# Performance work log

Hardware: AMD Instinct MI355X
Metric: run time of the kernel (lower is better)

Reference implementation:

```python
import jax, jax.numpy as jnp
import numpy as np

NUM_LEVELS = 3
BASE_SCALE = 0.25
RES = 3
TRUNC_K = 128
KNN = 32
EPS = 1e-5


def group_norm(x, w, b, groups):
    # x: [B, C, *spatial]
    B, C = x.shape[0], x.shape[1]
    xr = x.reshape(B, groups, -1)
    m = xr.mean(-1, keepdims=True)
    v = xr.var(-1, keepdims=True)
    xn = ((xr - m) * jax.lax.rsqrt(v + EPS)).reshape(x.shape)
    bshape = (1, C) + (1,) * (x.ndim - 2)
    return xn * w.reshape(bshape) + b.reshape(bshape)


def prelu(x, a):
    return jnp.where(x >= 0, x, a * x)


def setup_inputs() -> dict:
    key = jax.random.key(0)
    ks = jax.random.split(key, 12)
    b, dim, n = 2, 128, 8192
    inp = {
        'fmap1': jax.random.normal(ks[0], (b, dim, n), jnp.float32),
        'fmap2': jax.random.normal(ks[1], (b, dim, n), jnp.float32),
        'xyz2': jax.random.normal(ks[2], (b, n, 3), jnp.float32),
        'coords': jax.random.normal(ks[3], (b, n, 3), jnp.float32),
        # out_conv: Conv1d(81,128,1) -> GN(8,128) -> PReLU -> Conv1d(128,64,1)
        'oc_w1': jax.random.normal(ks[4], (128, RES ** 3 * NUM_LEVELS), jnp.float32) * 0.05,
        'oc_b1': jnp.zeros((128,), jnp.float32),
        'oc_gn_w': jnp.ones((128,), jnp.float32),
        'oc_gn_b': jnp.zeros((128,), jnp.float32),
        'oc_prelu': jnp.asarray(0.25, jnp.float32),
        'oc_w2': jax.random.normal(ks[5], (64, 128), jnp.float32) * 0.05,
        'oc_b2': jnp.zeros((64,), jnp.float32),
        # knn_conv: Conv2d(4,64,1) -> GN(8,64) -> PReLU
        'kc_w': jax.random.normal(ks[6], (64, 4), jnp.float32) * 0.1,
        'kc_b': jnp.zeros((64,), jnp.float32),
        'kc_gn_w': jnp.ones((64,), jnp.float32),
        'kc_gn_b': jnp.zeros((64,), jnp.float32),
        'kc_prelu': jnp.asarray(0.25, jnp.float32),
        # knn_out: Conv1d(64,64,1)
        'ko_w': jax.random.normal(ks[7], (64, 64), jnp.float32) * 0.05,
        'ko_b': jnp.zeros((64,), jnp.float32),
    }
    return inp


def _forward(fmap1, fmap2, xyz2, coords,
             oc_w1, oc_b1, oc_gn_w, oc_gn_b, oc_prelu, oc_w2, oc_b2,
             kc_w, kc_b, kc_gn_w, kc_gn_b, kc_prelu, ko_w, ko_b):
    b, dim, n1 = fmap1.shape
    # --- init_module: correlation + top-k truncation ---
    corr = jnp.einsum('bdm,bdn->bmn', fmap1, fmap2) / jnp.sqrt(jnp.asarray(dim, jnp.float32))
    tcorr, idx = jax.lax.top_k(corr, TRUNC_K)           # [b,n1,K]
    txyz = jax.vmap(lambda pts, i: pts[i])(xyz2, idx)   # [b,n1,K,3]

    # --- voxel feature: per-level histogram scatter-add with count normalization ---
    half = np.floor(RES / 2)
    feats = []
    for lvl in range(NUM_LEVELS):
        r = BASE_SCALE * 2 ** lvl
        dv = jnp.round((txyz - coords[:, :, None, :]) / r)               # [b,n1,K,3]
        valid = jnp.all(jnp.abs(dv) <= half, axis=-1)                     # [b,n1,K] bool
        dv = dv + 1.0
        cube = (dv[..., 0] * RES ** 2 + dv[..., 1] * RES + dv[..., 2]).astype(jnp.int32)
        cube = jax.lax.stop_gradient(cube * valid)                        # invalid -> bin 0
        vmask = jax.lax.stop_gradient(valid.astype(tcorr.dtype))
        onehot = jax.nn.one_hot(cube, RES ** 3, dtype=tcorr.dtype)        # [b,n1,K,27]
        corr_add = jnp.einsum('bnk,bnkc->bnc', tcorr * vmask, onehot)
        corr_cnt = jnp.clip(jnp.einsum('bnk,bnkc->bnc', vmask, onehot), 1.0, float(n1))
        feats.append(jnp.transpose(corr_add / corr_cnt, (0, 2, 1)))       # [b,27,n1]
    vox = jnp.concatenate(feats, axis=1)                                  # [b,81,n1]
    h = jnp.einsum('oc,bcn->bon', oc_w1, vox) + oc_b1[None, :, None]
    h = prelu(group_norm(h, oc_gn_w, oc_gn_b, 8), oc_prelu)
    vox_feat = jnp.einsum('oc,bcn->bon', oc_w2, h) + oc_b2[None, :, None]  # [b,64,n1]

    # --- knn feature: nearest truncated correspondences, conv, max-pool ---
    diff = txyz - coords[:, :, None, :]
    dist = jnp.sum(diff * diff, axis=-1)                                  # [b,n1,K]
    _, nbr = jax.lax.top_k(-dist, KNN)                                    # [b,n1,knn]
    knn_corr = jnp.take_along_axis(tcorr, nbr, axis=2)[:, None]           # [b,1,n1,knn]
    knn_xyz = jnp.take_along_axis(txyz, nbr[..., None], axis=2)           # [b,n1,knn,3]
    knn_xyz = jnp.transpose(knn_xyz, (0, 3, 1, 2)) - jnp.transpose(coords, (0, 2, 1))[..., None]
    kin = jnp.concatenate([knn_corr, knn_xyz], axis=1)                    # [b,4,n1,knn]
    kf = jnp.einsum('oc,bcnk->bonk', kc_w, kin) + kc_b[None, :, None, None]
    kf = prelu(group_norm(kf, kc_gn_w, kc_gn_b, 8), kc_prelu)
    kf = jnp.max(kf, axis=3)                                              # [b,64,n1]
    knn_feat = jnp.einsum('oc,bcn->bon', ko_w, kf) + ko_b[None, :, None]

    return vox_feat + knn_feat                                            # [b,64,n1]


def reference(fmap1, fmap2, xyz2, coords,
              oc_w1, oc_b1, oc_gn_w, oc_gn_b, oc_prelu, oc_w2, oc_b2,
              kc_w, kc_b, kc_gn_w, kc_gn_b, kc_prelu, ko_w, ko_b):
    return _forward(fmap1, fmap2, xyz2, coords,
                    oc_w1, oc_b1, oc_gn_w, oc_gn_b, oc_prelu, oc_w2, oc_b2,
                    kc_w, kc_b, kc_gn_w, kc_gn_b, kc_prelu, ko_w, ko_b)
```

## Files before the change

### kernel.cpp

```cpp
#include <hip/hip_runtime.h>

#define NN 8192
#define TK 128
#define KNNK 32
#define CAP 352
#define CSTR 353

typedef unsigned long long u64;
typedef long long i64;
typedef unsigned int u32;
typedef unsigned short u16;
typedef _Float16 f16;
typedef __attribute__((ext_vector_type(8))) _Float16 half8;
typedef __attribute__((ext_vector_type(4))) float f32x4;


union HU { u16 u; f16 f; };
__device__ __forceinline__ u16 f2h_bits(float v){ HU h; h.f = (f16)v; return h.u; }
__device__ __forceinline__ float h2f(u16 u){ HU h; h.u = u; return (float)h.f; }

__device__ __forceinline__ u32 f2key(float v){
    u32 u = __float_as_uint(v);
    return u ^ ((u32)((int)u >> 31) | 0x80000000u);
}
__device__ __forceinline__ float key2f(u32 k){
    u32 u = (k & 0x80000000u) ? (k ^ 0x80000000u) : ~k;
    return __uint_as_float(u);
}

__global__ void k0_zero(u64* __restrict__ stats){
    const int t = threadIdx.x;
    if (t < 72) stats[t] = 0ull;
}

__global__ __launch_bounds__(256) void k0b_pack(const float* __restrict__ src,
                                                f16* __restrict__ pl){
    const int tid = blockIdx.x*256 + threadIdx.x;
    const int n  = tid & (NN-1);
    const int kg = (tid >> 13) & 15;
    const int b  = tid >> 17;
    const float* s = src + ((size_t)(b*128 + kg*8))*NN + n;
    u32 hw[4], lw[4];
    #pragma unroll
    for (int p=0; p<4; ++p){
        const float v0 = s[(2*p  )*NN], v1 = s[(2*p+1)*NN];
        const u16 h0 = f2h_bits(v0), h1 = f2h_bits(v1);
        const float r0 = (v0 - h2f(h0))*1024.f, r1 = (v1 - h2f(h1))*1024.f;
        hw[p] = (u32)h0 | ((u32)h1 << 16);
        lw[p] = (u32)f2h_bits(r0) | ((u32)f2h_bits(r1) << 16);
    }
    const size_t o = 2*((size_t)(b*16 + kg)*NN + n);
    ((uint4*)pl)[o]   = make_uint4(hw[0],hw[1],hw[2],hw[3]);
    ((uint4*)pl)[o+1] = make_uint4(lw[0],lw[1],lw[2],lw[3]);
}

#define MFMA16(a,b,c) __builtin_amdgcn_mfma_f32_16x16x32_f16(a,b,c,0,0,0)

__global__ __launch_bounds__(1024, 2) void k1_corr_topk(
    const float* __restrict__ fmap1, const f16* __restrict__ f2p,
    const float* __restrict__ xyz2, const float* __restrict__ coords,
    const float* __restrict__ w1, const float* __restrict__ b1,
    u16* __restrict__ wsh, uint2* __restrict__ wskin, u64* __restrict__ stats)
{
    __shared__ u64   ckey[32][CSTR];
    __shared__ float sdist[32][128];
    __shared__ u64   vboth[32][81];
    __shared__ float voxn[32][81];
    __shared__ int   ccnt[32];
    __shared__ float rsig[32];
    __shared__ u64   wgo[8], wgq[8], wk1[4], wk2[16];

    const int t = threadIdx.x;
    const int lane = t & 63, wv = t >> 6;
    const int blk = blockIdx.x;
    const int b = (blk >> 2) & 1;
    const int i0 = (((blk & 3) << 6) | (blk >> 3)) * 32;

    if (t < 32) ccnt[t] = 0;
    if (t < 8){ wgo[t]=0ull; wgq[t]=0ull; }
    if (t < 4) wk1[t]=0ull;
    if (t < 16) wk2[t]=0ull;
    for (int z=t; z<32*81; z+=1024) ((u64*)vboth)[z]=0ull;

    const float scl = 0.08838834764831845f;

    half8 Ah[2][4], Al[2][4];
    float nrm[2] = {0.f, 0.f};
    const float* f1b = fmap1 + (size_t)b*128*NN;
    #pragma unroll
    for (int g=0; g<2; ++g){
        const int row = i0 + g*16 + (lane & 15);
        #pragma unroll
        for (int s=0; s<4; ++s){
            const int kb = s*32 + (lane>>4)*8;
            #pragma unroll
            for (int j=0; j<8; ++j){
                const float v = f1b[(size_t)(kb+j)*NN + row];
                const f16 h = (f16)v;
                Ah[g][s][j] = h;
                Al[g][s][j] = (f16)((v - (float)h)*1024.f);
                nrm[g] = fmaf(v, v, nrm[g]);
            }
        }
    }
    #pragma unroll
    for (int g=0; g<2; ++g){
        nrm[g] += __shfl_xor(nrm[g], 16);
        nrm[g] += __shfl_xor(nrm[g], 32);
    }
    if (wv == 0 && lane < 16){
        rsig[lane]      = fmaxf(sqrtf(nrm[0])*scl, 1e-20f);
        rsig[16 + lane] = fmaxf(sqrtf(nrm[1])*scl, 1e-20f);
    }
    __syncthreads();

    float rth[2][4];
    #pragma unroll
    for (int g=0; g<2; ++g)
        #pragma unroll
        for (int q=0; q<4; ++q)
            rth[g][q] = 1.9f * rsig[g*16 + (lane>>4)*4 + q];

    const f16* Bp = f2p + (size_t)b*16*NN*16;
    for (int ch=0; ch<16; ++ch){
        const int colbase = ch*512 + wv*32;
        #pragma unroll
        for (int tl=0; tl<2; ++tl){
            f32x4 Cm0=(f32x4)0.f, Cm1=(f32x4)0.f, Cl0=(f32x4)0.f, Cl1=(f32x4)0.f;
            const int col = colbase + tl*16 + (lane & 15);
            #pragma unroll
            for (int s=0; s<4; ++s){
                const int kg = s*4 + (lane>>4);
                const size_t off = ((size_t)kg*NN + col)*16;
                const half8 bh = *(const half8*)(Bp + off);
                const half8 bl = *(const half8*)(Bp + off + 8);
                Cm0 = MFMA16(Ah[0][s], bh, Cm0);
                Cl0 = MFMA16(Al[0][s], bh, Cl0);
                Cl0 = MFMA16(Ah[0][s], bl, Cl0);
                Cm1 = MFMA16(Ah[1][s], bh, Cm1);
                Cl1 = MFMA16(Al[1][s], bh, Cl1);
                Cl1 = MFMA16(Ah[1][s], bl, Cl1);
            }
            #pragma unroll
            for (int q=0; q<4; ++q){
                const float v0 = (Cm0[q] + Cl0[q]*(1.f/1024.f)) * scl;
                if (v0 > rth[0][q]){
                    const int r = (lane>>4)*4 + q;
                    const u64 key = ((u64)f2key(v0) << 13) | (u64)(8191 - col);
                    const int slot = atomicAdd(&ccnt[r], 1);
                    if (slot < CAP) ckey[r][slot] = key;
                }
                const float v1 = (Cm1[q] + Cl1[q]*(1.f/1024.f)) * scl;
                if (v1 > rth[1][q]){
                    const int r = 16 + (lane>>4)*4 + q;
                    const u64 key = ((u64)f2key(v1) << 13) | (u64)(8191 - col);
                    const int slot = atomicAdd(&ccnt[r], 1);
                    if (slot < CAP) ckey[r][slot] = key;
                }
            }
        }
    }
    __syncthreads();

    {
        const int r = t >> 5, s = t & 31;
        const int cnt = min(ccnt[r], CAP);
        u64 mkey[11]; int mrank[11];
        #pragma unroll
        for (int u=0; u<11; ++u){
            const int idx = s + (u<<5);
            mkey[u] = ckey[r][idx];
            mrank[u] = (idx < cnt) ? 0 : TK;
        }
        for (int j=0; j<cnt; ++j){
            const u64 kj = ckey[r][j];
            #pragma unroll
            for (int u=0; u<11; ++u)
                mrank[u] += (kj > mkey[u]) ? 1 : 0;
        }
        __syncthreads();
        #pragma unroll
        for (int u=0; u<11; ++u){
            if (mrank[u] < TK) ckey[r][mrank[u]] = mkey[u];
        }
    }
    __syncthreads();

    float wdx[8], wdy[8], wdz[8], wvl[8];
    float w1r[21];
    if (t >= 512){
        const int r = (t-512) >> 4, s = (t-512) & 15;
        const int i = i0 + r;
        const float cx = coords[((size_t)b*NN + i)*3 + 0];
        const float cy = coords[((size_t)b*NN + i)*3 + 1];
        const float cz = coords[((size_t)b*NN + i)*3 + 2];
        #pragma unroll
        for (int u=0; u<8; ++u){
            const int w = s + u*16;
            const u64 key = ckey[r][w];
            const int col = 8191 - (int)(key & 8191u);
            const float val = key2f((u32)(key >> 13));
            const float* pp = xyz2 + ((size_t)b*NN + col)*3;
            const float dx = pp[0]-cx, dy = pp[1]-cy, dz = pp[2]-cz;
            sdist[r][w] = dx*dx + dy*dy + dz*dz;
            wdx[u]=dx; wdy[u]=dy; wdz[u]=dz; wvl[u]=val;
            #pragma unroll
            for (int lvl=0; lvl<3; ++lvl){
                const float rs = 0.25f * (float)(1<<lvl);
                const float fx = rintf(dx/rs), fy = rintf(dy/rs), fz = rintf(dz/rs);
                if (fabsf(fx)<=1.f && fabsf(fy)<=1.f && fabsf(fz)<=1.f){
                    const int bin = lvl*27 + ((int)fx+1)*9 + ((int)fy+1)*3 + ((int)fz+1);
                    atomicAdd(&vboth[r][bin], (1ull<<40) | (u64)llrintf(val*67108864.f));
                }
            }
        }
    } else {
        #pragma unroll
        for (int u=0; u<21; ++u){
            const int idx = t + (u<<9);
            if (idx < 128*81) w1r[u] = w1[idx];
        }
    }
    __syncthreads();

    float* w1s = (float*)&ckey[0][0];
    if (t < 512){
        #pragma unroll
        for (int u=0; u<21; ++u){
            const int idx = t + (u<<9);
            if (idx < 128*81) w1s[idx] = w1r[u];
        }
        for (int z=t; z<32*81; z+=512){
            const u64 k = ((u64*)vboth)[z];
            const float vv = (float)(k & ((1ull<<40)-1)) * (1.f/67108864.f);
            const float c = fmaxf((float)(u32)(k >> 40), 1.f);
            ((float*)voxn)[z] = vv / c;
        }
    } else {
        const int r = (t-512) >> 4, s = (t-512) & 15;
        const int i = i0 + r;
        float my[8]; int rank[8];
        #pragma unroll
        for (int u=0; u<8; ++u){ my[u] = sdist[r][s + u*16]; rank[u] = 0; }
        for (int v2=0; v2<128; ++v2){
            const float o = sdist[r][v2];
            #pragma unroll
            for (int u=0; u<8; ++u)
                rank[u] += (o < my[u] || (o == my[u] && v2 < s + u*16)) ? 1 : 0;
        }
        float m1[4] = {0.f,0.f,0.f,0.f};
        float m2[16];
        #pragma unroll
        for (int q=0;q<16;q++) m2[q]=0.f;
        #pragma unroll
        for (int u=0; u<8; ++u){
            if (rank[u] < KNNK){
                const float kv[4] = {wvl[u], wdx[u], wdy[u], wdz[u]};
                uint2 kw;
                kw.x = (u32)f2h_bits(kv[0]) | ((u32)f2h_bits(kv[1]) << 16);
                kw.y = (u32)f2h_bits(kv[2]) | ((u32)f2h_bits(kv[3]) << 16);
                wskin[((size_t)b*NN + i)*KNNK + rank[u]] = kw;
                #pragma unroll
                for (int a2=0;a2<4;a2++){
                    m1[a2] += kv[a2];
                    #pragma unroll
                    for (int b2=0;b2<4;b2++) m2[a2*4+b2] += kv[a2]*kv[b2];
                }
            }
        }
        #pragma unroll
        for (int q=0; q<20; ++q){
            i64 v = llrintf(((q<4) ? m1[q] : m2[q-4]) * 1048576.f);
            #pragma unroll
            for (int off=1; off<64; off<<=1) v += __shfl_xor(v, off);
            if (lane == 0){
                if (q < 4) atomicAdd(&wk1[q], (u64)v);
                else       atomicAdd(&wk2[q-4], (u64)v);
            }
        }
    }
    __syncthreads();

    if (t < 512){
        const int r = t >> 4, cg = t & 15;
        const int i = i0 + r;
        float h8[8];
        #pragma unroll
        for (int i2=0;i2<8;i2++) h8[i2] = b1[cg*8+i2];
        for (int j=0; j<81; ++j){
            const float vj = voxn[r][j];
            #pragma unroll
            for (int i2=0;i2<8;i2++) h8[i2] = fmaf(w1s[(cg*8+i2)*81 + j], vj, h8[i2]);
        }
        uint4 hv4;
        hv4.x = (u32)f2h_bits(h8[0]) | ((u32)f2h_bits(h8[1])<<16);
        hv4.y = (u32)f2h_bits(h8[2]) | ((u32)f2h_bits(h8[3])<<16);
        hv4.z = (u32)f2h_bits(h8[4]) | ((u32)f2h_bits(h8[5])<<16);
        hv4.w = (u32)f2h_bits(h8[6]) | ((u32)f2h_bits(h8[7])<<16);
        ((uint4*)wsh)[((size_t)(b*NN + i)*128 + cg*8) >> 3] = hv4;
        i64 s1 = 0, s2 = 0;
        #pragma unroll
        for (int i2=0;i2<8;i2++){
            s1 += llrintf(h8[i2]*1048576.f);
            s2 += llrintf(h8[i2]*h8[i2]*1048576.f);
        }
        s1 += __shfl_xor(s1, 1);  s2 += __shfl_xor(s2, 1);
        s1 += __shfl_xor(s1, 16); s2 += __shfl_xor(s2, 16);
        s1 += __shfl_xor(s1, 32); s2 += __shfl_xor(s2, 32);
        if (((lane & 1) == 0) && (lane >> 4) == 0){
            atomicAdd(&wgo[cg>>1], (u64)s1);
            atomicAdd(&wgq[cg>>1], (u64)s2);
        }
    }
    __syncthreads();

    if (t < 8){ atomicAdd(&stats[b*8 + t], wgo[t]); atomicAdd(&stats[16 + b*8 + t], wgq[t]); }
    if (t < 4){ atomicAdd(&stats[32 + b*4 + t], wk1[t]); }
    if (t < 16){ atomicAdd(&stats[40 + b*16 + t], wk2[t]); }
}

__global__ void k2_stats(const u64* __restrict__ stats, float* __restrict__ fstats,
                         const float* __restrict__ kcw, const float* __restrict__ kcb)
{
    const int t = threadIdx.x;
    if (t < 16){
        const double S = (double)(i64)stats[t];
        const double Q = (double)(i64)stats[16+t];
        const double cnt = 16.0*8192.0;
        const double mean = S / 1048576.0 / cnt;
        const double var  = Q / 1048576.0 / cnt - mean*mean;
        fstats[t]    = (float)mean;
        fstats[16+t] = (float)(1.0/sqrt(var + 1e-5));
    }
    if (t >= 32 && t < 48){
        const int u = t - 32;
        const int b = u >> 3, g = u & 7;
        double M1[4], M2[4][4];
        for (int a=0;a<4;a++) M1[a] = (double)(i64)stats[32 + b*4 + a] / 1048576.0;
        for (int a=0;a<4;a++) for (int c=0;c<4;c++)
            M2[a][c] = (double)(i64)stats[40 + b*16 + a*4 + c] / 1048576.0;
        const double cnt = 8192.0*32.0;
        double SUM=0.0, SSQ=0.0;
        for (int c = g*8; c < g*8+8; ++c){
            double wv[4]; for (int a=0;a<4;a++) wv[a] = (double)kcw[c*4+a];
            const double bc = (double)kcb[c];
            double sc = bc*cnt, qc = bc*bc*cnt;
            for (int a=0;a<4;a++){
                sc += wv[a]*M1[a];
                qc += 2.0*bc*wv[a]*M1[a];
                for (int e=0;e<4;e++) qc += wv[a]*wv[e]*M2[a][e];
            }
            SUM += sc; SSQ += qc;
        }
        const double denom = 8.0*cnt;
        const double mean = SUM/denom;
        const double var  = SSQ/denom - mean*mean;
        fstats[32+u] = (float)mean;
        fstats[48+u] = (float)(1.0/sqrt(var + 1e-5));
    }
}

__global__ __launch_bounds__(256) void k3a_vox(
    const u16* __restrict__ wsh, const float* __restrict__ fstats,
    const float* __restrict__ gnw, const float* __restrict__ gnb,
    const float* __restrict__ pr, const float* __restrict__ w2,
    const float* __restrict__ b2, float* __restrict__ out)
{
    __shared__ float p[16][128];
    __shared__ float w2s[64][129];
    const int t = threadIdx.x;
    const int base = blockIdx.x * 16;
    const int b = base >> 13;
    for (int u=t; u<64*128; u+=256) w2s[u>>7][u&127] = w2[u];
    const float a = pr[0];
    for (int u=t; u<16*128; u+=256){
        const int pt=u>>7, c=u&127, g=c>>4;
        const float hv = h2f(wsh[(size_t)(base+pt)*128 + c]);
        const float hn = (hv - fstats[b*8+g])*fstats[16+b*8+g]*gnw[c] + gnb[c];
        p[pt][c] = hn>=0.f ? hn : a*hn;
    }
    __syncthreads();
    const int o = t & 63, wv = t >> 6;
    float acc0=b2[o], acc1=acc0, acc2=acc0, acc3=acc0;
    for (int c=0;c<128;c++){
        const float w = w2s[o][c];
        acc0 = fmaf(w, p[wv*4+0][c], acc0);
        acc1 = fmaf(w, p[wv*4+1][c], acc1);
        acc2 = fmaf(w, p[wv*4+2][c], acc2);
        acc3 = fmaf(w, p[wv*4+3][c], acc3);
    }
    const float4 res = {acc0,acc1,acc2,acc3};
    *(float4*)&out[((size_t)b*64 + o)*NN + (base & (NN-1)) + wv*4] = res;
}

__global__ __launch_bounds__(256) void k3b_knn(
    const uint2* __restrict__ wskin, const float* __restrict__ fstats,
    const float* __restrict__ kcw, const float* __restrict__ kcb,
    const float* __restrict__ gnw, const float* __restrict__ gnb,
    const float* __restrict__ pr, const float* __restrict__ kow,
    const float* __restrict__ kob, float* __restrict__ out)
{
    __shared__ float skin[16][KNNK*4+4];
    __shared__ float kml[16][65];
    __shared__ float kos[64][65];
    const int t = threadIdx.x;
    const int base = blockIdx.x * 16;
    const int b = base >> 13;
    for (int v=t; v<16*KNNK; v+=256){
        const int pt = v>>5, q = v&31;
        const uint2 kw = wskin[(size_t)(base+pt)*KNNK + q];
        skin[pt][q*4+0] = h2f((u16)(kw.x & 0xFFFF));
        skin[pt][q*4+1] = h2f((u16)(kw.x >> 16));
        skin[pt][q*4+2] = h2f((u16)(kw.y & 0xFFFF));
        skin[pt][q*4+3] = h2f((u16)(kw.y >> 16));
    }
    for (int u=t; u<4096; u+=256) kos[u>>6][u&63] = kow[u];
    __syncthreads();
    const float a = pr[0];
    {
        const int pt = t>>4, cb = (t&15)*4;
        #pragma unroll
        for (int cc=0; cc<4; ++cc){
            const int c = cb+cc, g = c>>3;
            const float mean = fstats[32+b*8+g], rstd = fstats[48+b*8+g];
            const float gw = rstd*gnw[c], gb = gnb[c]-mean*gw;
            const float w0=kcw[c*4], w1v=kcw[c*4+1], w2v=kcw[c*4+2], w3=kcw[c*4+3], bc=kcb[c];
            float mx = -3.0e38f;
            for (int kk=0;kk<KNNK;kk++){
                const float4 sv = *(const float4*)&skin[pt][kk*4];
                float kf = fmaf(w0,sv.x, fmaf(w1v,sv.y, fmaf(w2v,sv.z, fmaf(w3,sv.w, bc))));
                float hn = kf*gw + gb;
                hn = hn>=0.f ? hn : a*hn;
                mx = fmaxf(mx, hn);
            }
            kml[pt][c] = mx;
        }
    }
    __syncthreads();
    const int o = t & 63, wv = t >> 6;
    float acc0=kob[o], acc1=acc0, acc2=acc0, acc3=acc0;
    for (int c=0;c<64;c++){
        const float w = kos[o][c];
        acc0 = fmaf(w, kml[wv*4+0][c], acc0);
        acc1 = fmaf(w, kml[wv*4+1][c], acc1);
        acc2 = fmaf(w, kml[wv*4+2][c], acc2);
        acc3 = fmaf(w, kml[wv*4+3][c], acc3);
    }
    float* op = &out[((size_t)b*64 + o)*NN + (base & (NN-1)) + wv*4];
    float4 cur = *(float4*)op;
    cur.x += acc0; cur.y += acc1; cur.z += acc2; cur.w += acc3;
    *(float4*)op = cur;
}

extern "C" void kernel_launch(void* const* d_in, const int* in_sizes, int n_in,
                              void* d_out, int out_size, void* d_ws, size_t ws_size,
                              hipStream_t stream)
{
    const float* fmap1   = (const float*)d_in[0];
    const float* fmap2   = (const float*)d_in[1];
    const float* xyz2    = (const float*)d_in[2];
    const float* coords  = (const float*)d_in[3];
    const float* oc_w1   = (const float*)d_in[4];
    const float* oc_b1   = (const float*)d_in[5];
    const float* oc_gn_w = (const float*)d_in[6];
    const float* oc_gn_b = (const float*)d_in[7];
    const float* oc_pr   = (const float*)d_in[8];
    const float* oc_w2   = (const float*)d_in[9];
    const float* oc_b2   = (const float*)d_in[10];
    const float* kc_w    = (const float*)d_in[11];
    const float* kc_b    = (const float*)d_in[12];
    const float* kc_gn_w = (const float*)d_in[13];
    const float* kc_gn_b = (const float*)d_in[14];
    const float* kc_pr   = (const float*)d_in[15];
    const float* ko_w    = (const float*)d_in[16];
    const float* ko_b    = (const float*)d_in[17];

    char* ws = (char*)d_ws;
    f16*   f2p    = (f16*)ws;
    u16*   wsh    = (u16*)(ws + (size_t)8*1024*1024);
    uint2* wskin  = (uint2*)(ws + (size_t)12*1024*1024);
    u64*   stats  = (u64*) (ws + (size_t)16*1024*1024);
    float* fstats = (float*)(ws + (size_t)16*1024*1024 + 1024);
    float* out    = (float*)d_out;

    k0_zero<<<dim3(1), dim3(128), 0, stream>>>(stats);
    k0b_pack<<<dim3(1024), dim3(256), 0, stream>>>(fmap2, f2p);
    k1_corr_topk<<<dim3(512), dim3(1024), 0, stream>>>(
        fmap1, f2p, xyz2, coords, oc_w1, oc_b1, wsh, wskin, stats);
    k2_stats<<<dim3(1), dim3(64), 0, stream>>>(stats, fstats, kc_w, kc_b);
    k3a_vox<<<dim3(1024), dim3(256), 0, stream>>>(
        wsh, fstats, oc_gn_w, oc_gn_b, oc_pr, oc_w2, oc_b2, out);
    k3b_knn<<<dim3(1024), dim3(256), 0, stream>>>(
        wskin, fstats, kc_w, kc_b, kc_gn_w, kc_gn_b, kc_pr, ko_w, ko_b, out);
}
```

Before: 358.2 us.

## Replace rank-sort top-k with radix threshold search, compaction and small sort

The per-row top-128 selection used to rank every candidate (up to 352) against all others. It now finds the 128th-largest key with a bitwise radix search that counts across the row's lanes using wave shuffles. It then compacts the survivors with a prefix sum and rank-sorts only those 128 keys. The candidate threshold is also pre-divided by the scale, so the scale multiply only runs for keys that pass. The sort now leans on wavefront lockstep instead of a barrier between reads and writes, and it assumes at least 128 candidates per row.

```diff
diff --git a/kernel.cpp b/kernel.cpp
--- a/kernel.cpp
+++ b/kernel.cpp
@@ -114,12 +114,12 @@
     }
     __syncthreads();
 
-    float rth[2][4];
+    float rthr[2][4];
     #pragma unroll
     for (int g=0; g<2; ++g)
         #pragma unroll
         for (int q=0; q<4; ++q)
-            rth[g][q] = 1.9f * rsig[g*16 + (lane>>4)*4 + q];
+            rthr[g][q] = 1.9f * rsig[g*16 + (lane>>4)*4 + q] / scl;
 
     const f16* Bp = f2p + (size_t)b*16*NN*16;
     for (int ch=0; ch<16; ++ch){
@@ -143,17 +143,17 @@
             }
             #pragma unroll
             for (int q=0; q<4; ++q){
-                const float v0 = (Cm0[q] + Cl0[q]*(1.f/1024.f)) * scl;
-                if (v0 > rth[0][q]){
+                const float r0 = fmaf(Cl0[q], (1.f/1024.f), Cm0[q]);
+                if (r0 > rthr[0][q]){
                     const int r = (lane>>4)*4 + q;
-                    const u64 key = ((u64)f2key(v0) << 13) | (u64)(8191 - col);
+                    const u64 key = ((u64)f2key(r0*scl) << 13) | (u64)(8191 - col);
                     const int slot = atomicAdd(&ccnt[r], 1);
                     if (slot < CAP) ckey[r][slot] = key;
                 }
-                const float v1 = (Cm1[q] + Cl1[q]*(1.f/1024.f)) * scl;
-                if (v1 > rth[1][q]){
+                const float r1 = fmaf(Cl1[q], (1.f/1024.f), Cm1[q]);
+                if (r1 > rthr[1][q]){
                     const int r = 16 + (lane>>4)*4 + q;
-                    const u64 key = ((u64)f2key(v1) << 13) | (u64)(8191 - col);
+                    const u64 key = ((u64)f2key(r1*scl) << 13) | (u64)(8191 - col);
                     const int slot = atomicAdd(&ccnt[r], 1);
                     if (slot < CAP) ckey[r][slot] = key;
                 }
@@ -165,24 +165,47 @@
     {
         const int r = t >> 5, s = t & 31;
         const int cnt = min(ccnt[r], CAP);
-        u64 mkey[11]; int mrank[11];
+        u64 mkey[11];
         #pragma unroll
         for (int u=0; u<11; ++u){
             const int idx = s + (u<<5);
-            mkey[u] = ckey[r][idx];
-            mrank[u] = (idx < cnt) ? 0 : TK;
-        }
-        for (int j=0; j<cnt; ++j){
+            const u64 k = ckey[r][idx];
+            mkey[u] = (idx < cnt) ? k : 0ull;
+        }
+        u64 T = 1ull << 44;
+        for (int bit = 43; bit >= 0; --bit){
+            const u64 cand = T | (1ull << bit);
+            int c = 0;
+            #pragma unroll
+            for (int u=0; u<11; ++u) c += (mkey[u] >= cand) ? 1 : 0;
+            c += __shfl_xor(c, 1); c += __shfl_xor(c, 2); c += __shfl_xor(c, 4);
+            c += __shfl_xor(c, 8); c += __shfl_xor(c, 16);
+            if (c >= TK) T = cand;
+        }
+        int mycnt = 0;
+        #pragma unroll
+        for (int u=0; u<11; ++u) mycnt += (mkey[u] >= T) ? 1 : 0;
+        int pre = mycnt;
+        #pragma unroll
+        for (int off=1; off<32; off<<=1){
+            const int v = __shfl_up(pre, off, 32);
+            if (s >= off) pre += v;
+        }
+        int base = pre - mycnt;
+        #pragma unroll
+        for (int u=0; u<11; ++u){
+            if (mkey[u] >= T){ ckey[r][base] = mkey[u]; ++base; }
+        }
+        u64 rk[4]; int rr[4];
+        #pragma unroll
+        for (int u2=0; u2<4; ++u2){ rk[u2] = ckey[r][s + (u2<<5)]; rr[u2] = 0; }
+        for (int j=0; j<TK; ++j){
             const u64 kj = ckey[r][j];
             #pragma unroll
-            for (int u=0; u<11; ++u)
-                mrank[u] += (kj > mkey[u]) ? 1 : 0;
-        }
-        __syncthreads();
-        #pragma unroll
-        for (int u=0; u<11; ++u){
-            if (mrank[u] < TK) ckey[r][mrank[u]] = mkey[u];
-        }
+            for (int u2=0; u2<4; ++u2) rr[u2] += (kj > rk[u2]) ? 1 : 0;
+        }
+        #pragma unroll
+        for (int u2=0; u2<4; ++u2) ckey[r][rr[u2]] = rk[u2];
     }
     __syncthreads();
 
```

Result: faster. 316.5 us (-11.7%).
